# Kernel tuning notes

Hardware: AMD Instinct MI355X
Metric: run time of the kernel (lower is better)

Reference implementation:

```python
import jax, jax.numpy as jnp
import numpy as np

H = 512  # hidden_size


def setup_inputs() -> dict:
    key = jax.random.key(0)
    ks = jax.random.split(key, 8)
    B, L_tgt, L_src = 4, 32, 1024
    query = jax.random.normal(ks[0], (B, L_tgt, H), dtype=jnp.float32)
    states = jax.random.normal(ks[1], (B, L_src, 2 * H), dtype=jnp.float32)
    source_mask = jnp.ones((B, L_src), dtype=jnp.int32)
    s = 0.02
    Wq = jax.random.normal(ks[2], (H, 2 * H), dtype=jnp.float32) * s      # _linear_query.weight^T
    bq = jax.random.normal(ks[3], (2 * H,), dtype=jnp.float32) * s        # _linear_query.bias
    Ws = jax.random.normal(ks[4], (2 * H, 2 * H), dtype=jnp.float32) * s  # _linear_source.weight^T (no bias)
    v = jax.random.normal(ks[5], (2 * H,), dtype=jnp.float32) * s         # _v.weight (no bias)
    Wc = jax.random.normal(ks[6], (3 * H, H), dtype=jnp.float32) * s      # _context.weight^T
    bc = jax.random.normal(ks[7], (H,), dtype=jnp.float32) * s            # _context.bias
    return {"query": query, "states": states, "source_mask": source_mask,
            "Wq": Wq, "bq": bq, "Ws": Ws, "v": v, "Wc": Wc, "bc": bc}


def reference(query, states, source_mask, Wq, bq, Ws, v, Wc, bc):
    # Bahdanau additive attention.
    # query: (B, T, H), states: (B, S, 2H), source_mask: (B, S)
    qf = query @ Wq + bq                         # (B, T, 2H)
    sf = states @ Ws                             # (B, S, 2H)
    # alignments: v . tanh(qf[:, :, None] + sf[:, None, :])  -> (B, T, S)
    feats = jnp.tanh(qf[:, :, None, :] + sf[:, None, :, :])  # (B, T, S, 2H)
    alignments = jnp.einsum('btsd,d->bts', feats, v)
    # mask (B, S) -> (B, 1, S); masked positions get -inf before softmax
    alignments = jnp.where(source_mask[:, None, :].astype(bool), alignments, -jnp.inf)
    attentions = jax.nn.softmax(alignments, axis=2)           # (B, T, S)
    context = jnp.einsum('bts,bsd->btd', attentions, states)  # (B, T, 2H)
    concat_context = jnp.concatenate((context, query), axis=2)  # (B, T, 3H)
    attention_hidden = concat_context @ Wc + bc               # (B, T, H)
    attentions_t = jnp.swapaxes(attentions, 1, 2)             # (B, S, T)
    return (context, attention_hidden, attentions_t)
```

## Files before the change

kernel.cpp:

```cpp
#include <hip/hip_runtime.h>
#include <math.h>


typedef unsigned short u16;
typedef __bf16 bf16x8 __attribute__((ext_vector_type(8)));
typedef float floatx4 __attribute__((ext_vector_type(4)));

#define B_ 4
#define T_ 32
#define S_ 1024
#define H_ 512
#define D_ 1024
#define BT_ 128
#define TWO_LOG2E 2.8853900817779268f

__device__ __forceinline__ float bf2f(u16 u) {
  unsigned int i = ((unsigned int)u) << 16;
  return __builtin_bit_cast(float, i);
}
__device__ __forceinline__ u16 f2bf(float f) {
  unsigned int i = __builtin_bit_cast(unsigned int, f);
  i += 0x7fffu + ((i >> 16) & 1u);
  return (u16)(i >> 16);
}
__device__ __forceinline__ void ld_g2l_16(const u16* g, u16* l) {
  __builtin_amdgcn_global_load_lds((__attribute__((address_space(1))) void*)(u16*)g,
                                   (__attribute__((address_space(3))) void*)l, 16, 0, 0);
}


__global__ __launch_bounds__(256) void prep_fused(const float* __restrict__ states, const float* __restrict__ Ws,
                                                  const float* __restrict__ query, const float* __restrict__ Wq,
                                                  const float* __restrict__ bq,
                                                  u16* __restrict__ sbf, u16* __restrict__ sbfT,
                                                  u16* __restrict__ WsT, float* __restrict__ qf) {
  __shared__ u16 tile[32][65];
  __shared__ float q[8][128];
  const int t = threadIdx.x;
  if (blockIdx.x < 512) {
    const int n0 = (blockIdx.x & 15) * 64, k0 = (blockIdx.x >> 4) * 32;
    const int kr = t >> 3, nc = (t & 7) * 8;
    const float* p = Ws + (size_t)(k0 + kr) * D_ + n0 + nc;
    float4 a = *(const float4*)p, b = *(const float4*)(p + 4);
    tile[kr][nc + 0] = f2bf(a.x); tile[kr][nc + 1] = f2bf(a.y);
    tile[kr][nc + 2] = f2bf(a.z); tile[kr][nc + 3] = f2bf(a.w);
    tile[kr][nc + 4] = f2bf(b.x); tile[kr][nc + 5] = f2bf(b.y);
    tile[kr][nc + 6] = f2bf(b.z); tile[kr][nc + 7] = f2bf(b.w);
    __syncthreads();
    const int nr = t >> 2, kc = (t & 3) * 8;
    union { uint4 v; u16 s[8]; } st;
#pragma unroll
    for (int i = 0; i < 8; ++i) st.s[i] = tile[kc + i][nr];
    *(uint4*)(WsT + (size_t)(n0 + nr) * D_ + k0 + kc) = st.v;
  } else if (blockIdx.x < 2560) {
    const int bid = blockIdx.x - 512;
    const int b = bid >> 9;
    const int r2 = bid & 511;
    const int d0 = (r2 & 15) * 64, s0 = (r2 >> 4) * 32;
    const int sr = t >> 3, dc = (t & 7) * 8;
    const float* p = states + ((size_t)b * S_ + s0 + sr) * D_ + d0 + dc;
    float4 a = *(const float4*)p, bb = *(const float4*)(p + 4);
    union { uint4 v; u16 s[8]; } pk;
    pk.s[0] = f2bf(a.x); pk.s[1] = f2bf(a.y); pk.s[2] = f2bf(a.z); pk.s[3] = f2bf(a.w);
    pk.s[4] = f2bf(bb.x); pk.s[5] = f2bf(bb.y); pk.s[6] = f2bf(bb.z); pk.s[7] = f2bf(bb.w);
    *(uint4*)(sbf + ((size_t)b * S_ + s0 + sr) * D_ + d0 + dc) = pk.v;
#pragma unroll
    for (int i = 0; i < 8; ++i) tile[sr][dc + i] = pk.s[i];
    __syncthreads();
    const int dr = t >> 2, sc = (t & 3) * 8;
    union { uint4 v; u16 s[8]; } st;
#pragma unroll
    for (int i = 0; i < 8; ++i) st.s[i] = tile[sc + i][dr];
    *(uint4*)(sbfT + ((size_t)b * D_ + d0 + dr) * S_ + s0 + sc) = st.v;
  } else {
    const int idx = blockIdx.x - 2560;
    const int c0 = (idx & 3) * 256, r0 = ((idx >> 2) & 15) * 8, k0 = (idx >> 6) * 128;
    for (int i = t; i < 8 * 128; i += 256) {
      const int rl = i >> 7, kk = i & 127;
      q[rl][kk] = query[(size_t)(r0 + rl) * H_ + k0 + kk];
    }
    __syncthreads();
    const int col = c0 + t;
    float acc[8] = {};
    for (int kk = 0; kk < 128; ++kk) {
      const float w = Wq[(size_t)(k0 + kk) * D_ + col];
#pragma unroll
      for (int r = 0; r < 8; ++r) acc[r] = fmaf(q[r][kk], w, acc[r]);
    }
    const float bb = (k0 == 0) ? bq[col] : 0.f;
#pragma unroll
    for (int r = 0; r < 8; ++r)
      atomicAdd(&qf[(size_t)(r0 + r) * D_ + col], TWO_LOG2E * (acc[r] + bb));
  }
}

__global__ __launch_bounds__(256) void f2e_sfgemm(const u16* __restrict__ A, const u16* __restrict__ BT,
                                                  u16* __restrict__ Cb) {
  __shared__ __align__(16) u16 sA[128 * 64];
  __shared__ __align__(16) u16 sB[64 * 64];
  const int bm0 = blockIdx.y * 128, bn0 = blockIdx.x * 64;
  const int t = threadIdx.x;
  const int wv = t >> 6, lane = t & 63;
  const int wm = (wv >> 1) * 64, wn = (wv & 1) * 32;
  const int fm = lane & 15, fq = lane >> 4;
  const int srow = lane >> 3, sp = lane & 7;

  floatx4 acc[4][2];
  const floatx4 fz = {0.f, 0.f, 0.f, 0.f};
#pragma unroll
  for (int i = 0; i < 4; ++i) { acc[i][0] = fz; acc[i][1] = fz; }

  for (int k0 = 0; k0 < D_; k0 += 64) {
    __syncthreads();
#pragma unroll
    for (int j = 0; j < 4; ++j) {
      const int r = wv * 32 + j * 8 + srow;
      const int c = sp ^ (r & 7);
      ld_g2l_16(A + (size_t)(bm0 + r) * D_ + k0 + c * 8, &sA[(wv * 32 + j * 8) * 64]);
    }
#pragma unroll
    for (int j = 0; j < 2; ++j) {
      const int r = wv * 16 + j * 8 + srow;
      const int c = sp ^ (r & 7);
      ld_g2l_16(BT + (size_t)(bn0 + r) * D_ + k0 + c * 8, &sB[(wv * 16 + j * 8) * 64]);
    }
    __syncthreads();
#pragma unroll
    for (int win = 0; win < 2; ++win) {
      bf16x8 af[4], bfr[2];
#pragma unroll
      for (int i = 0; i < 4; ++i) {
        const int R = wm + i * 16 + fm;
        af[i] = *(const bf16x8*)&sA[R * 64 + ((win * 4 + fq) ^ (R & 7)) * 8];
      }
#pragma unroll
      for (int j = 0; j < 2; ++j) {
        const int R = wn + j * 16 + fm;
        bfr[j] = *(const bf16x8*)&sB[R * 64 + ((win * 4 + fq) ^ (R & 7)) * 8];
      }
#pragma unroll
      for (int i = 0; i < 4; ++i)
#pragma unroll
        for (int j = 0; j < 2; ++j)
          acc[i][j] = __builtin_amdgcn_mfma_f32_16x16x32_bf16(af[i], bfr[j], acc[i][j], 0, 0, 0);
    }
  }
#pragma unroll
  for (int i = 0; i < 4; ++i)
#pragma unroll
    for (int j = 0; j < 2; ++j)
#pragma unroll
      for (int r = 0; r < 4; ++r) {
        const int row = bm0 + wm + i * 16 + fq * 4 + r;
        const int col = bn0 + wn + j * 16 + fm;
        Cb[(size_t)row * D_ + col] = f2bf(TWO_LOG2E * acc[i][j][r]);
      }
}

__global__ __launch_bounds__(256, 6) void f3f_align(const float* __restrict__ qf, const u16* __restrict__ sfb,
                                                    const float* __restrict__ v, float* __restrict__ alg) {
  const int wid = (blockIdx.x * 256 + threadIdx.x) >> 6;
  const int lane = threadIdx.x & 63;
  const int b = wid >> 10, s = wid & 1023;
  const int t0 = blockIdx.y * 16;
  float vr[16], sr[16];
  {
    union { uint4 v[2]; u16 s[16]; } u;
    const uint4* sp = (const uint4*)(sfb + (size_t)wid * D_ + lane * 16);
    u.v[0] = sp[0]; u.v[1] = sp[1];
    const float* vp = v + lane * 16;
#pragma unroll
    for (int c = 0; c < 4; ++c) {
      float4 w = *(const float4*)(vp + 4 * c);
      vr[4 * c + 0] = w.x; vr[4 * c + 1] = w.y; vr[4 * c + 2] = w.z; vr[4 * c + 3] = w.w;
    }
#pragma unroll
    for (int j = 0; j < 16; ++j) sr[j] = bf2f(u.s[j]);
  }
  float sum[16];
#pragma unroll
  for (int tt = 0; tt < 16; ++tt) sum[tt] = 0.f;

  const float* qbase = qf + ((size_t)(b * T_ + t0)) * D_ + lane * 16;
  for (int tt = 0; tt < 16; ++tt) {
    const float4* qp = (const float4*)(qbase + (size_t)tt * D_);
    float acc = 0.f;
#pragma unroll
    for (int c = 0; c < 4; ++c) {
      float4 q4 = qp[c];
      float xs[4] = {q4.x, q4.y, q4.z, q4.w};
#pragma unroll
      for (int u2 = 0; u2 < 4; ++u2) {
        const int j = 4 * c + u2;
        const float x = xs[u2] + sr[j];
        const float e = __builtin_amdgcn_exp2f(x);
        acc = fmaf(vr[j], fmaf(-2.f, __builtin_amdgcn_rcpf(e + 1.f), 1.f), acc);
      }
    }
    sum[tt] = acc;
  }
#pragma unroll
  for (int off = 32; off > 0; off >>= 1)
#pragma unroll
    for (int tt = 0; tt < 16; ++tt) sum[tt] += __shfl_xor(sum[tt], off);
  if (lane == 0) {
#pragma unroll
    for (int tt = 0; tt < 16; ++tt)
      alg[((size_t)(b * T_ + t0 + tt)) * S_ + s] = sum[tt];
  }
}

__global__ __launch_bounds__(256) void f4b_softmax(const float* __restrict__ alg, const int* __restrict__ mask,
                                                   float* __restrict__ out_at, u16* __restrict__ pbf) {
  const int r = blockIdx.x;
  const int b = r >> 5, t = r & 31;
  const int tid = threadIdx.x;
  __shared__ float red[256];
  float a[4];
#pragma unroll
  for (int jj = 0; jj < 4; ++jj) {
    const int s = tid + 256 * jj;
    const float x = alg[(size_t)r * S_ + s];
    a[jj] = (mask[(size_t)b * S_ + s] != 0) ? x : -3.0e38f;
  }
  float m = fmaxf(fmaxf(a[0], a[1]), fmaxf(a[2], a[3]));
  red[tid] = m; __syncthreads();
  for (int st = 128; st > 0; st >>= 1) { if (tid < st) red[tid] = fmaxf(red[tid], red[tid + st]); __syncthreads(); }
  m = red[0]; __syncthreads();
  float e[4], lsum = 0.f;
#pragma unroll
  for (int jj = 0; jj < 4; ++jj) {
    e[jj] = (a[jj] > -1.0e38f) ? expf(a[jj] - m) : 0.f;
    lsum += e[jj];
  }
  red[tid] = lsum; __syncthreads();
  for (int st = 128; st > 0; st >>= 1) { if (tid < st) red[tid] += red[tid + st]; __syncthreads(); }
  const float rs = 1.f / red[0];
#pragma unroll
  for (int jj = 0; jj < 4; ++jj) {
    const int s = tid + 256 * jj;
    const float p = e[jj] * rs;
    out_at[((size_t)b * S_ + s) * T_ + t] = p;
    pbf[(size_t)r * S_ + s] = f2bf(p);
  }
}

__global__ __launch_bounds__(256) void f5c_context(const u16* __restrict__ pbf, const u16* __restrict__ sbfT,
                                                   float* __restrict__ ctx) {
  const int b = blockIdx.x >> 4, dt = blockIdx.x & 15;
  const int wv = threadIdx.x >> 6, lane = threadIdx.x & 63;
  const int n0 = dt * 64 + wv * 16;
  const int fm = lane & 15, fq = lane >> 4;
  const floatx4 fz = {0.f, 0.f, 0.f, 0.f};
  floatx4 acc0 = fz, acc1 = fz;
  const u16* pa0 = pbf + ((size_t)b * T_ + fm) * S_ + fq * 8;
  const u16* pa1 = pbf + ((size_t)b * T_ + 16 + fm) * S_ + fq * 8;
  const u16* pb  = sbfT + ((size_t)b * D_ + n0 + fm) * S_ + fq * 8;
#pragma unroll 4
  for (int k0 = 0; k0 < S_; k0 += 32) {
    bf16x8 a0 = *(const bf16x8*)(pa0 + k0);
    bf16x8 a1 = *(const bf16x8*)(pa1 + k0);
    bf16x8 bb = *(const bf16x8*)(pb + k0);
    acc0 = __builtin_amdgcn_mfma_f32_16x16x32_bf16(a0, bb, acc0, 0, 0, 0);
    acc1 = __builtin_amdgcn_mfma_f32_16x16x32_bf16(a1, bb, acc1, 0, 0, 0);
  }
  const int col = n0 + fm;
#pragma unroll
  for (int r = 0; r < 4; ++r) {
    ctx[((size_t)b * T_ + fq * 4 + r) * D_ + col] = acc0[r];
    ctx[((size_t)b * T_ + 16 + fq * 4 + r) * D_ + col] = acc1[r];
  }
}

__global__ __launch_bounds__(256) void f6b_outproj(const float* __restrict__ ctx, const float* __restrict__ query,
                                                   const float* __restrict__ Wc, const float* __restrict__ bc,
                                                   float* __restrict__ out_hid) {
  __shared__ float cq[16][128];
  const int c0 = blockIdx.x * 128, r0 = blockIdx.y * 16, k0 = blockIdx.z * 128;
  const int tid = threadIdx.x;
  const int cl = tid & 127, rh = tid >> 7;
  for (int i = tid; i < 16 * 128; i += 256) {
    const int rl = i >> 7, kk = i & 127;
    const int k = k0 + kk, row = r0 + rl;
    cq[rl][kk] = (k < D_) ? ctx[(size_t)row * D_ + k] : query[(size_t)row * H_ + k - D_];
  }
  __syncthreads();
  float acc[8] = {};
  for (int kk = 0; kk < 128; ++kk) {
    const float w = Wc[(size_t)(k0 + kk) * H_ + c0 + cl];
#pragma unroll
    for (int rr = 0; rr < 8; ++rr) acc[rr] = fmaf(cq[rh * 8 + rr][kk], w, acc[rr]);
  }
  const float bb = (blockIdx.z == 0) ? bc[c0 + cl] : 0.f;
#pragma unroll
  for (int rr = 0; rr < 8; ++rr)
    atomicAdd(&out_hid[(size_t)(r0 + rh * 8 + rr) * H_ + c0 + cl], acc[rr] + bb);
}


__global__ __launch_bounds__(256) void kc_cvt(const float* __restrict__ in, u16* __restrict__ out) {
  const size_t i0 = ((size_t)blockIdx.x * 256 + threadIdx.x) * 8;
  float4 a = *(const float4*)(in + i0);
  float4 b = *(const float4*)(in + i0 + 4);
  union { uint4 v; u16 s[8]; } r;
  r.s[0] = f2bf(a.x); r.s[1] = f2bf(a.y); r.s[2] = f2bf(a.z); r.s[3] = f2bf(a.w);
  r.s[4] = f2bf(b.x); r.s[5] = f2bf(b.y); r.s[6] = f2bf(b.z); r.s[7] = f2bf(b.w);
  *(uint4*)(out + i0) = r.v;
}

__global__ __launch_bounds__(256) void f0_transpose(const float* __restrict__ Ws, u16* __restrict__ WsT) {
  __shared__ u16 tile[32][65];
  const int n0 = blockIdx.x * 64, k0 = blockIdx.y * 32;
  const int t = threadIdx.x;
  {
    const int kr = t >> 3, nc = (t & 7) * 8;
    const float* p = Ws + (size_t)(k0 + kr) * D_ + n0 + nc;
    float4 a = *(const float4*)p, b = *(const float4*)(p + 4);
    tile[kr][nc + 0] = f2bf(a.x); tile[kr][nc + 1] = f2bf(a.y);
    tile[kr][nc + 2] = f2bf(a.z); tile[kr][nc + 3] = f2bf(a.w);
    tile[kr][nc + 4] = f2bf(b.x); tile[kr][nc + 5] = f2bf(b.y);
    tile[kr][nc + 6] = f2bf(b.z); tile[kr][nc + 7] = f2bf(b.w);
  }
  __syncthreads();
  {
    const int nr = t >> 2, kc = (t & 3) * 8;
    union { uint4 v; u16 s[8]; } st;
#pragma unroll
    for (int i = 0; i < 8; ++i) st.s[i] = tile[kc + i][nr];
    *(uint4*)(WsT + (size_t)(n0 + nr) * D_ + k0 + kc) = st.v;
  }
}

__global__ __launch_bounds__(256) void f1b_qf(const float* __restrict__ query, const float* __restrict__ Wq,
                                              const float* __restrict__ bq, float* __restrict__ qf) {
  __shared__ float q[8][128];
  const int c0 = blockIdx.x * 256, r0 = blockIdx.y * 8, k0 = blockIdx.z * 128;
  const int tid = threadIdx.x;
  for (int i = tid; i < 8 * 128; i += 256) {
    const int rl = i >> 7, kk = i & 127;
    q[rl][kk] = query[(size_t)(r0 + rl) * H_ + k0 + kk];
  }
  __syncthreads();
  const int col = c0 + tid;
  float acc[8] = {};
  for (int kk = 0; kk < 128; ++kk) {
    const float w = Wq[(size_t)(k0 + kk) * D_ + col];
#pragma unroll
    for (int r = 0; r < 8; ++r) acc[r] = fmaf(q[r][kk], w, acc[r]);
  }
  const float bb = (blockIdx.z == 0) ? bq[col] : 0.f;
#pragma unroll
  for (int r = 0; r < 8; ++r)
    atomicAdd(&qf[(size_t)(r0 + r) * D_ + col], TWO_LOG2E * (acc[r] + bb));
}

__global__ __launch_bounds__(256) void f2c_sfgemm(const u16* __restrict__ A, const u16* __restrict__ BT,
                                                  u16* __restrict__ Cb) {
  __shared__ __align__(16) u16 sA[128 * 40];
  __shared__ __align__(16) u16 sB[64 * 40];
  const int bm0 = blockIdx.y * 128, bn0 = blockIdx.x * 64;
  const int t = threadIdx.x;
  const int wv = t >> 6, lane = t & 63;
  const int wm = (wv >> 1) * 64, wn = (wv & 1) * 32;
  const int fm = lane & 15, fq = lane >> 4;
  const int arow = t >> 1, akc = (t & 1) * 16;
  const int brow = t >> 2, bkc = (t & 3) * 8;
  floatx4 acc[4][2];
  const floatx4 fz = {0.f, 0.f, 0.f, 0.f};
#pragma unroll
  for (int i = 0; i < 4; ++i) { acc[i][0] = fz; acc[i][1] = fz; }
  const uint4* gA = (const uint4*)(A + (size_t)(bm0 + arow) * D_ + akc);
  const uint4* gB = (const uint4*)(BT + (size_t)(bn0 + brow) * D_ + bkc);
  for (int k0 = 0; k0 < D_; k0 += 32) {
    uint4 va0 = gA[k0 >> 3];
    uint4 va1 = gA[(k0 >> 3) + 1];
    uint4 vb = gB[k0 >> 3];
    __syncthreads();
    *(uint4*)&sA[arow * 40 + akc] = va0;
    *(uint4*)&sA[arow * 40 + akc + 8] = va1;
    *(uint4*)&sB[brow * 40 + bkc] = vb;
    __syncthreads();
    bf16x8 af[4], bfr[2];
#pragma unroll
    for (int i = 0; i < 4; ++i) af[i] = *(const bf16x8*)&sA[(wm + i * 16 + fm) * 40 + fq * 8];
#pragma unroll
    for (int j = 0; j < 2; ++j) bfr[j] = *(const bf16x8*)&sB[(wn + j * 16 + fm) * 40 + fq * 8];
#pragma unroll
    for (int i = 0; i < 4; ++i)
#pragma unroll
      for (int j = 0; j < 2; ++j)
        acc[i][j] = __builtin_amdgcn_mfma_f32_16x16x32_bf16(af[i], bfr[j], acc[i][j], 0, 0, 0);
  }
#pragma unroll
  for (int i = 0; i < 4; ++i)
#pragma unroll
    for (int j = 0; j < 2; ++j)
#pragma unroll
      for (int r = 0; r < 4; ++r) {
        const int row = bm0 + wm + i * 16 + fq * 4 + r;
        const int col = bn0 + wn + j * 16 + fm;
        Cb[(size_t)row * D_ + col] = f2bf(TWO_LOG2E * acc[i][j][r]);
      }
}

__global__ __launch_bounds__(256) void f2d_sfgemm(const float* __restrict__ A, const u16* __restrict__ BT,
                                                  u16* __restrict__ Cb) {
  __shared__ __align__(16) u16 sA[128 * 40];
  __shared__ __align__(16) u16 sB[64 * 40];
  const int bm0 = blockIdx.y * 128, bn0 = blockIdx.x * 64;
  const int t = threadIdx.x;
  const int wv = t >> 6, lane = t & 63;
  const int wm = (wv >> 1) * 64, wn = (wv & 1) * 32;
  const int fm = lane & 15, fq = lane >> 4;
  const int arow = t >> 1, akc = (t & 1) * 16;
  const int brow = t >> 2, bkc = (t & 3) * 8;
  floatx4 acc[4][2];
  const floatx4 fz = {0.f, 0.f, 0.f, 0.f};
#pragma unroll
  for (int i = 0; i < 4; ++i) { acc[i][0] = fz; acc[i][1] = fz; }
  const float* gA = A + (size_t)(bm0 + arow) * D_ + akc;
  const uint4* gB = (const uint4*)(BT + (size_t)(bn0 + brow) * D_ + bkc);
  for (int k0 = 0; k0 < D_; k0 += 32) {
    float4 a0 = *(const float4*)(gA + k0);
    float4 a1 = *(const float4*)(gA + k0 + 4);
    float4 a2 = *(const float4*)(gA + k0 + 8);
    float4 a3 = *(const float4*)(gA + k0 + 12);
    uint4 vb = gB[k0 >> 3];
    union { uint4 v[2]; u16 s[16]; } pa;
    pa.s[0] = f2bf(a0.x); pa.s[1] = f2bf(a0.y); pa.s[2] = f2bf(a0.z); pa.s[3] = f2bf(a0.w);
    pa.s[4] = f2bf(a1.x); pa.s[5] = f2bf(a1.y); pa.s[6] = f2bf(a1.z); pa.s[7] = f2bf(a1.w);
    pa.s[8] = f2bf(a2.x); pa.s[9] = f2bf(a2.y); pa.s[10] = f2bf(a2.z); pa.s[11] = f2bf(a2.w);
    pa.s[12] = f2bf(a3.x); pa.s[13] = f2bf(a3.y); pa.s[14] = f2bf(a3.z); pa.s[15] = f2bf(a3.w);
    __syncthreads();
    *(uint4*)&sA[arow * 40 + akc] = pa.v[0];
    *(uint4*)&sA[arow * 40 + akc + 8] = pa.v[1];
    *(uint4*)&sB[brow * 40 + bkc] = vb;
    __syncthreads();
    bf16x8 af[4], bfr[2];
#pragma unroll
    for (int i = 0; i < 4; ++i) af[i] = *(const bf16x8*)&sA[(wm + i * 16 + fm) * 40 + fq * 8];
#pragma unroll
    for (int j = 0; j < 2; ++j) bfr[j] = *(const bf16x8*)&sB[(wn + j * 16 + fm) * 40 + fq * 8];
#pragma unroll
    for (int i = 0; i < 4; ++i)
#pragma unroll
      for (int j = 0; j < 2; ++j)
        acc[i][j] = __builtin_amdgcn_mfma_f32_16x16x32_bf16(af[i], bfr[j], acc[i][j], 0, 0, 0);
  }
#pragma unroll
  for (int i = 0; i < 4; ++i)
#pragma unroll
    for (int j = 0; j < 2; ++j)
#pragma unroll
      for (int r = 0; r < 4; ++r) {
        const int row = bm0 + wm + i * 16 + fq * 4 + r;
        const int col = bn0 + wn + j * 16 + fm;
        Cb[(size_t)row * D_ + col] = f2bf(TWO_LOG2E * acc[i][j][r]);
      }
}

__global__ __launch_bounds__(256) void f4_softmax(const float* __restrict__ alg, const int* __restrict__ mask,
                                                  float* __restrict__ attn) {
  const int r = blockIdx.x;
  const int b = r >> 5;
  const int tid = threadIdx.x;
  __shared__ float red[256];
  float a[4];
#pragma unroll
  for (int jj = 0; jj < 4; ++jj) {
    const int s = tid + 256 * jj;
    const float x = alg[(size_t)r * S_ + s];
    a[jj] = (mask[(size_t)b * S_ + s] != 0) ? x : -3.0e38f;
  }
  float m = fmaxf(fmaxf(a[0], a[1]), fmaxf(a[2], a[3]));
  red[tid] = m; __syncthreads();
  for (int st = 128; st > 0; st >>= 1) { if (tid < st) red[tid] = fmaxf(red[tid], red[tid + st]); __syncthreads(); }
  m = red[0]; __syncthreads();
  float e[4], lsum = 0.f;
#pragma unroll
  for (int jj = 0; jj < 4; ++jj) {
    e[jj] = (a[jj] > -1.0e38f) ? expf(a[jj] - m) : 0.f;
    lsum += e[jj];
  }
  red[tid] = lsum; __syncthreads();
  for (int st = 128; st > 0; st >>= 1) { if (tid < st) red[tid] += red[tid + st]; __syncthreads(); }
  const float rs = 1.f / red[0];
#pragma unroll
  for (int jj = 0; jj < 4; ++jj)
    attn[(size_t)r * S_ + tid + 256 * jj] = e[jj] * rs;
}

__global__ __launch_bounds__(256) void f5b_context(const float* __restrict__ attn, const u16* __restrict__ sbf,
                                                   float* __restrict__ ctx, float* __restrict__ out_at) {
  __shared__ float at[16][64];
  const int s0 = blockIdx.x * 64, t0 = blockIdx.y * 16, b = blockIdx.z;
  const int tid = threadIdx.x;
  for (int i = tid; i < 16 * 64; i += 256) {
    const int tl = i >> 6, sl = i & 63;
    at[tl][sl] = attn[(size_t)(b * T_ + t0 + tl) * S_ + s0 + sl];
  }
  __syncthreads();
  for (int i = tid; i < 64 * 16; i += 256) {
    const int sl = i >> 4, tl = i & 15;
    out_at[((size_t)b * S_ + s0 + sl) * T_ + t0 + tl] = at[tl][sl];
  }
  float acc[16][4] = {};
  for (int sl = 0; sl < 64; ++sl) {
    const u16* srow = sbf + ((size_t)b * S_ + s0 + sl) * D_ + tid;
    float sv[4];
#pragma unroll
    for (int jj = 0; jj < 4; ++jj) sv[jj] = bf2f(srow[256 * jj]);
#pragma unroll
    for (int tl = 0; tl < 16; ++tl) {
      const float w = at[tl][sl];
#pragma unroll
      for (int jj = 0; jj < 4; ++jj) acc[tl][jj] = fmaf(w, sv[jj], acc[tl][jj]);
    }
  }
#pragma unroll
  for (int tl = 0; tl < 16; ++tl)
#pragma unroll
    for (int jj = 0; jj < 4; ++jj)
      atomicAdd(&ctx[(size_t)(b * T_ + t0 + tl) * D_ + tid + 256 * jj], acc[tl][jj]);
}

__global__ __launch_bounds__(256) void f5_context(const float* __restrict__ attn, const float* __restrict__ states,
                                                  float* __restrict__ ctx, float* __restrict__ out_at) {
  __shared__ float at[16][64];
  const int s0 = blockIdx.x * 64, t0 = blockIdx.y * 16, b = blockIdx.z;
  const int tid = threadIdx.x;
  for (int i = tid; i < 16 * 64; i += 256) {
    const int tl = i >> 6, sl = i & 63;
    at[tl][sl] = attn[(size_t)(b * T_ + t0 + tl) * S_ + s0 + sl];
  }
  __syncthreads();
  for (int i = tid; i < 64 * 16; i += 256) {
    const int sl = i >> 4, tl = i & 15;
    out_at[((size_t)b * S_ + s0 + sl) * T_ + t0 + tl] = at[tl][sl];
  }
  float acc[16][4] = {};
  for (int sl = 0; sl < 64; ++sl) {
    const float* srow = states + ((size_t)b * S_ + s0 + sl) * D_ + tid;
    float sv[4];
#pragma unroll
    for (int jj = 0; jj < 4; ++jj) sv[jj] = srow[256 * jj];
#pragma unroll
    for (int tl = 0; tl < 16; ++tl) {
      const float w = at[tl][sl];
#pragma unroll
      for (int jj = 0; jj < 4; ++jj) acc[tl][jj] = fmaf(w, sv[jj], acc[tl][jj]);
    }
  }
#pragma unroll
  for (int tl = 0; tl < 16; ++tl)
#pragma unroll
    for (int jj = 0; jj < 4; ++jj)
      atomicAdd(&ctx[(size_t)(b * T_ + t0 + tl) * D_ + tid + 256 * jj], acc[tl][jj]);
}


__global__ __launch_bounds__(256) void k1_qf(const float* __restrict__ query, const float* __restrict__ Wq,
                                             const float* __restrict__ bq, float* __restrict__ qf) {
  const int r = blockIdx.x;
  const int tid = threadIdx.x;
  __shared__ float q[H_];
  for (int i = tid; i < H_; i += 256) q[i] = query[(size_t)r * H_ + i];
  __syncthreads();
#pragma unroll
  for (int jj = 0; jj < 4; ++jj) {
    const int j = tid + 256 * jj;
    float acc = bq[j];
    for (int k = 0; k < H_; ++k) acc = fmaf(q[k], Wq[(size_t)k * D_ + j], acc);
    qf[(size_t)r * D_ + j] = acc;
  }
}

__global__ __launch_bounds__(256) void k23_align(const float* __restrict__ states, const float* __restrict__ Ws,
                                                 const float* __restrict__ v, const float* __restrict__ qf,
                                                 float* __restrict__ alg) {
  const int b = blockIdx.x >> 6;
  const int s0 = (blockIdx.x & 63) * 16;
  const int tid = threadIdx.x, lane = tid & 63, wv = tid >> 6;
  __shared__ u16 stL[16 * D_];
  __shared__ float vvL[D_];
  __shared__ float red[16 * 4];
  for (int i = tid; i < 16 * D_; i += 256) {
    const int row = i >> 10, col = i & (D_ - 1);
    stL[i] = f2bf(states[((size_t)b * S_ + s0 + row) * D_ + col]);
  }
  for (int i = tid; i < D_; i += 256) vvL[i] = v[i];
  __syncthreads();
  float acc[64];
#pragma unroll
  for (int i = 0; i < 64; ++i) acc[i] = 0.f;
#pragma unroll 4
  for (int k = 0; k < D_; ++k) {
    float wsv[4];
#pragma unroll
    for (int jj = 0; jj < 4; ++jj) wsv[jj] = Ws[(size_t)k * D_ + tid + 256 * jj];
#pragma unroll
    for (int i = 0; i < 16; ++i) {
      const float sv = bf2f(stL[i * D_ + k]);
#pragma unroll
      for (int jj = 0; jj < 4; ++jj) acc[i * 4 + jj] = fmaf(sv, wsv[jj], acc[i * 4 + jj]);
    }
  }
  for (int t = 0; t < T_; ++t) {
    float qv[4];
#pragma unroll
    for (int jj = 0; jj < 4; ++jj) qv[jj] = qf[((size_t)b * T_ + t) * D_ + tid + 256 * jj];
    float part[16];
#pragma unroll
    for (int i = 0; i < 16; ++i) {
      float p = 0.f;
#pragma unroll
      for (int jj = 0; jj < 4; ++jj)
        p = fmaf(vvL[tid + 256 * jj], tanhf(qv[jj] + acc[i * 4 + jj]), p);
      part[i] = p;
    }
#pragma unroll
    for (int i = 0; i < 16; ++i) {
      float x = part[i];
#pragma unroll
      for (int off = 32; off > 0; off >>= 1) x += __shfl_xor(x, off);
      if (lane == 0) red[i * 4 + wv] = x;
    }
    __syncthreads();
    if (tid < 16)
      alg[((size_t)b * T_ + t) * S_ + s0 + tid] =
          red[tid * 4 + 0] + red[tid * 4 + 1] + red[tid * 4 + 2] + red[tid * 4 + 3];
    __syncthreads();
  }
}

__global__ __launch_bounds__(256) void k4_softmax(const float* __restrict__ alg, const int* __restrict__ mask,
                                                  float* __restrict__ attn) {
  const int r = blockIdx.x;
  const int b = r >> 5;
  const int tid = threadIdx.x;
  __shared__ float red[256];
  float a[4];
#pragma unroll
  for (int jj = 0; jj < 4; ++jj) {
    const int s = tid + 256 * jj;
    const float x = alg[(size_t)r * S_ + s];
    a[jj] = (mask[(size_t)b * S_ + s] != 0) ? x : -3.0e38f;
  }
  float m = fmaxf(fmaxf(a[0], a[1]), fmaxf(a[2], a[3]));
  red[tid] = m; __syncthreads();
  for (int st = 128; st > 0; st >>= 1) { if (tid < st) red[tid] = fmaxf(red[tid], red[tid + st]); __syncthreads(); }
  m = red[0]; __syncthreads();
  float e[4], lsum = 0.f;
#pragma unroll
  for (int jj = 0; jj < 4; ++jj) {
    e[jj] = (a[jj] > -1.0e38f) ? expf(a[jj] - m) : 0.f;
    lsum += e[jj];
  }
  red[tid] = lsum; __syncthreads();
  for (int st = 128; st > 0; st >>= 1) { if (tid < st) red[tid] += red[tid + st]; __syncthreads(); }
  const float rs = 1.f / red[0];
#pragma unroll
  for (int jj = 0; jj < 4; ++jj)
    attn[(size_t)r * S_ + tid + 256 * jj] = e[jj] * rs;
}

__global__ __launch_bounds__(256) void k56_ctx_proj(const float* __restrict__ attn, const float* __restrict__ states,
                                                    const float* __restrict__ query, const float* __restrict__ Wc,
                                                    const float* __restrict__ bc,
                                                    float* __restrict__ out_ctx, float* __restrict__ out_hid,
                                                    float* __restrict__ out_at) {
  const int r = blockIdx.x;
  const int b = r >> 5, t = r & (T_ - 1);
  const int tid = threadIdx.x;
  __shared__ float pr[S_];
  __shared__ float cq[D_ + H_];
  for (int s = tid; s < S_; s += 256) pr[s] = attn[(size_t)r * S_ + s];
  __syncthreads();
  for (int s = tid; s < S_; s += 256) out_at[((size_t)b * S_ + s) * T_ + t] = pr[s];
  float acc[4] = {0.f, 0.f, 0.f, 0.f};
  for (int s = 0; s < S_; ++s) {
    const float w = pr[s];
    const float* srow = states + ((size_t)b * S_ + s) * D_ + tid;
#pragma unroll
    for (int jj = 0; jj < 4; ++jj) acc[jj] = fmaf(w, srow[256 * jj], acc[jj]);
  }
#pragma unroll
  for (int jj = 0; jj < 4; ++jj) {
    cq[tid + 256 * jj] = acc[jj];
    out_ctx[(size_t)r * D_ + tid + 256 * jj] = acc[jj];
  }
  for (int i = tid; i < H_; i += 256) cq[D_ + i] = query[(size_t)r * H_ + i];
  __syncthreads();
#pragma unroll
  for (int jj = 0; jj < 2; ++jj) {
    const int n = tid + 256 * jj;
    float h = bc[n];
    for (int k = 0; k < D_ + H_; ++k) h = fmaf(cq[k], Wc[(size_t)k * H_ + n], h);
    out_hid[(size_t)r * H_ + n] = h;
  }
}

extern "C" void kernel_launch(void* const* d_in, const int* in_sizes, int n_in,
                              void* d_out, int out_size, void* d_ws, size_t ws_size,
                              hipStream_t stream) {
  const float* query  = (const float*)d_in[0];
  const float* states = (const float*)d_in[1];
  const int*   mask   = (const int*)d_in[2];
  const float* Wq     = (const float*)d_in[3];
  const float* bq     = (const float*)d_in[4];
  const float* Ws     = (const float*)d_in[5];
  const float* v      = (const float*)d_in[6];
  const float* Wc     = (const float*)d_in[7];
  const float* bc     = (const float*)d_in[8];

  float* A  = (float*)d_out;
  float* Bh = A + (size_t)BT_ * D_;
  float* C  = Bh + (size_t)BT_ * H_;

  char* ws = (char*)d_ws;
  u16*   sfb  = (u16*)(ws + 0);
  u16*   WsT  = (u16*)(ws + 8388608);
  float* alg  = (float*)(ws + 10485760);
  u16*   sbf  = (u16*)(ws + 11010048);
  u16*   sbfT = (u16*)(ws + 19398656);
  u16*   pbf  = (u16*)(ws + 27787264);

  const size_t WS_T1 = 11010048;
  const size_t WS_T2 = 19398656;
  const size_t WS_T3 = 28049408;

  if (ws_size >= WS_T3) {
    (void)hipMemsetAsync(A, 0, (size_t)(BT_ * D_ + BT_ * H_) * 4, stream);
    prep_fused<<<2816, 256, 0, stream>>>(states, Ws, query, Wq, bq, sbf, sbfT, WsT, A);
    f2e_sfgemm<<<dim3(16, 32), 256, 0, stream>>>(sbf, WsT, sfb);
    f3f_align<<<dim3(1024, 2), 256, 0, stream>>>(A, sfb, v, alg);
    f4b_softmax<<<BT_, 256, 0, stream>>>(alg, mask, C, pbf);
    f5c_context<<<64, 256, 0, stream>>>(pbf, sbfT, A);
    f6b_outproj<<<dim3(4, 8, 12), 256, 0, stream>>>(A, query, Wc, bc, Bh);
  } else if (ws_size >= WS_T1) {
    float* attn = alg;
    (void)hipMemsetAsync(A, 0, (size_t)(BT_ * D_ + BT_ * H_) * 4, stream);
    f1b_qf<<<dim3(4, 16, 4), 256, 0, stream>>>(query, Wq, bq, A);
    f0_transpose<<<dim3(16, 32), 256, 0, stream>>>(Ws, WsT);
    const int tier2 = (ws_size >= WS_T2);
    if (tier2) {
      kc_cvt<<<2048, 256, 0, stream>>>(states, sbf);
      f2c_sfgemm<<<dim3(16, 32), 256, 0, stream>>>(sbf, WsT, sfb);
    } else {
      f2d_sfgemm<<<dim3(16, 32), 256, 0, stream>>>(states, WsT, sfb);
    }
    f3f_align<<<dim3(1024, 2), 256, 0, stream>>>(A, sfb, v, C);
    (void)hipMemsetAsync(A, 0, (size_t)BT_ * D_ * 4, stream);
    f4_softmax<<<BT_, 256, 0, stream>>>(C, mask, attn);
    if (tier2)
      f5b_context<<<dim3(16, 2, 4), 256, 0, stream>>>(attn, sbf, A, C);
    else
      f5_context<<<dim3(16, 2, 4), 256, 0, stream>>>(attn, states, A, C);
    f6b_outproj<<<dim3(4, 8, 12), 256, 0, stream>>>(A, query, Wc, bc, Bh);
  } else {
    k1_qf<<<BT_, 256, 0, stream>>>(query, Wq, bq, A);
    k23_align<<<B_ * (S_ / 16), 256, 0, stream>>>(states, Ws, v, A, C);
    k4_softmax<<<BT_, 256, 0, stream>>>(C, mask, A);
    k56_ctx_proj<<<BT_, 256, 0, stream>>>(A, states, query, Wc, bc, A, Bh, C);
  }
}
```

Baseline: 186.3 us.

## Factor tanh into exponentials of query and source features to cut transcendentals

Adds a new top tier that precomputes exp(2*qf) and exp(2*sf) in the prep and GEMM epilogues. The alignment kernel then evaluates tanh(a+b) as 1 - 2/(e^a*e^b+1), so the inner loop needs one multiply and one reciprocal instead of a tanh per (t,s,d) element. This removes most transcendental work from the hot B*T*S*D loop. The cost is storing Es and Eq in fp32 instead of bf16, which needs more workspace and memory traffic, and the exponentials can overflow for large activations. It only runs when the workspace is large enough.

```diff
diff --git a/kernel.cpp b/kernel.cpp
--- a/kernel.cpp
+++ b/kernel.cpp
@@ -26,6 +26,216 @@
 __device__ __forceinline__ void ld_g2l_16(const u16* g, u16* l) {
   __builtin_amdgcn_global_load_lds((__attribute__((address_space(1))) void*)(u16*)g,
                                    (__attribute__((address_space(3))) void*)l, 16, 0, 0);
+}
+
+
+__global__ __launch_bounds__(256) void prep_fused2(const float* __restrict__ states, const float* __restrict__ Ws,
+                                                   const float* __restrict__ query, const float* __restrict__ Wq,
+                                                   const float* __restrict__ bq,
+                                                   u16* __restrict__ sbf, u16* __restrict__ sbfT,
+                                                   u16* __restrict__ WsT, float* __restrict__ Eq) {
+  __shared__ u16 tile[32][65];
+  __shared__ float qq[8 * 512];
+  const int t = threadIdx.x;
+  if (blockIdx.x < 512) {
+    const int n0 = (blockIdx.x & 15) * 64, k0 = (blockIdx.x >> 4) * 32;
+    const int kr = t >> 3, nc = (t & 7) * 8;
+    const float* p = Ws + (size_t)(k0 + kr) * D_ + n0 + nc;
+    float4 a = *(const float4*)p, b = *(const float4*)(p + 4);
+    tile[kr][nc + 0] = f2bf(a.x); tile[kr][nc + 1] = f2bf(a.y);
+    tile[kr][nc + 2] = f2bf(a.z); tile[kr][nc + 3] = f2bf(a.w);
+    tile[kr][nc + 4] = f2bf(b.x); tile[kr][nc + 5] = f2bf(b.y);
+    tile[kr][nc + 6] = f2bf(b.z); tile[kr][nc + 7] = f2bf(b.w);
+    __syncthreads();
+    const int nr = t >> 2, kc = (t & 3) * 8;
+    union { uint4 v; u16 s[8]; } st;
+#pragma unroll
+    for (int i = 0; i < 8; ++i) st.s[i] = tile[kc + i][nr];
+    *(uint4*)(WsT + (size_t)(n0 + nr) * D_ + k0 + kc) = st.v;
+  } else if (blockIdx.x < 2560) {
+    const int bid = blockIdx.x - 512;
+    const int b = bid >> 9;
+    const int r2 = bid & 511;
+    const int d0 = (r2 & 15) * 64, s0 = (r2 >> 4) * 32;
+    const int sr = t >> 3, dc = (t & 7) * 8;
+    const float* p = states + ((size_t)b * S_ + s0 + sr) * D_ + d0 + dc;
+    float4 a = *(const float4*)p, bb = *(const float4*)(p + 4);
+    union { uint4 v; u16 s[8]; } pk;
+    pk.s[0] = f2bf(a.x); pk.s[1] = f2bf(a.y); pk.s[2] = f2bf(a.z); pk.s[3] = f2bf(a.w);
+    pk.s[4] = f2bf(bb.x); pk.s[5] = f2bf(bb.y); pk.s[6] = f2bf(bb.z); pk.s[7] = f2bf(bb.w);
+    *(uint4*)(sbf + ((size_t)b * S_ + s0 + sr) * D_ + d0 + dc) = pk.v;
+#pragma unroll
+    for (int i = 0; i < 8; ++i) tile[sr][dc + i] = pk.s[i];
+    __syncthreads();
+    const int dr = t >> 2, sc = (t & 3) * 8;
+    union { uint4 v; u16 s[8]; } st;
+#pragma unroll
+    for (int i = 0; i < 8; ++i) st.s[i] = tile[sc + i][dr];
+    *(uint4*)(sbfT + ((size_t)b * D_ + d0 + dr) * S_ + s0 + sc) = st.v;
+  } else {
+    const int idx = blockIdx.x - 2560;
+    const int c0 = (idx & 3) * 256, r0 = (idx >> 2) * 8;
+    const float* qsrc = query + (size_t)r0 * H_;
+    for (int i = t; i < 1024; i += 256)
+      ((float4*)qq)[i] = ((const float4*)qsrc)[i];
+    __syncthreads();
+    const int col = c0 + t;
+    float acc[8] = {};
+    for (int kk = 0; kk < 512; kk += 4) {
+      const float w0 = Wq[(size_t)(kk + 0) * D_ + col];
+      const float w1 = Wq[(size_t)(kk + 1) * D_ + col];
+      const float w2 = Wq[(size_t)(kk + 2) * D_ + col];
+      const float w3 = Wq[(size_t)(kk + 3) * D_ + col];
+#pragma unroll
+      for (int r = 0; r < 8; ++r) {
+        const float4 q4 = *(const float4*)&qq[r * 512 + kk];
+        acc[r] = fmaf(q4.x, w0, acc[r]);
+        acc[r] = fmaf(q4.y, w1, acc[r]);
+        acc[r] = fmaf(q4.z, w2, acc[r]);
+        acc[r] = fmaf(q4.w, w3, acc[r]);
+      }
+    }
+    const float bb = bq[col];
+#pragma unroll
+    for (int r = 0; r < 8; ++r)
+      Eq[(size_t)(r0 + r) * D_ + col] = __builtin_amdgcn_exp2f(TWO_LOG2E * (acc[r] + bb));
+  }
+}
+
+__device__ __forceinline__ void f2f_stage(const u16* __restrict__ A, const u16* __restrict__ BT,
+                                          u16* sAb, u16* sBb, int bm0, int bn0, int k0,
+                                          int wv, int srow, int sp) {
+#pragma unroll
+  for (int j = 0; j < 4; ++j) {
+    const int r = wv * 32 + j * 8 + srow;
+    const int c = sp ^ (r & 7);
+    ld_g2l_16(A + (size_t)(bm0 + r) * D_ + k0 + c * 8, sAb + (wv * 32 + j * 8) * 64);
+  }
+#pragma unroll
+  for (int j = 0; j < 2; ++j) {
+    const int r = wv * 16 + j * 8 + srow;
+    const int c = sp ^ (r & 7);
+    ld_g2l_16(BT + (size_t)(bn0 + r) * D_ + k0 + c * 8, sBb + (wv * 16 + j * 8) * 64);
+  }
+}
+
+__device__ __forceinline__ void f2f_compute(const u16* sAb, const u16* sBb,
+                                            int wm, int wn, int fm, int fq, floatx4 (&acc)[4][2]) {
+#pragma unroll
+  for (int win = 0; win < 2; ++win) {
+    bf16x8 af[4], bfr[2];
+#pragma unroll
+    for (int i = 0; i < 4; ++i) {
+      const int R = wm + i * 16 + fm;
+      af[i] = *(const bf16x8*)&sAb[R * 64 + ((win * 4 + fq) ^ (R & 7)) * 8];
+    }
+#pragma unroll
+    for (int j = 0; j < 2; ++j) {
+      const int R = wn + j * 16 + fm;
+      bfr[j] = *(const bf16x8*)&sBb[R * 64 + ((win * 4 + fq) ^ (R & 7)) * 8];
+    }
+#pragma unroll
+    for (int i = 0; i < 4; ++i)
+#pragma unroll
+      for (int j = 0; j < 2; ++j)
+        acc[i][j] = __builtin_amdgcn_mfma_f32_16x16x32_bf16(af[i], bfr[j], acc[i][j], 0, 0, 0);
+  }
+}
+
+__global__ __launch_bounds__(256) void f2f_sfgemm(const u16* __restrict__ A, const u16* __restrict__ BT,
+                                                  float* __restrict__ Es) {
+  __shared__ __align__(16) u16 sA[2][128 * 64];
+  __shared__ __align__(16) u16 sB[2][64 * 64];
+  const int bm0 = blockIdx.y * 128, bn0 = blockIdx.x * 64;
+  const int t = threadIdx.x;
+  const int wv = t >> 6, lane = t & 63;
+  const int wm = (wv >> 1) * 64, wn = (wv & 1) * 32;
+  const int fm = lane & 15, fq = lane >> 4;
+  const int srow = lane >> 3, sp = lane & 7;
+
+  floatx4 acc[4][2];
+  const floatx4 fz = {0.f, 0.f, 0.f, 0.f};
+#pragma unroll
+  for (int i = 0; i < 4; ++i) { acc[i][0] = fz; acc[i][1] = fz; }
+
+  f2f_stage(A, BT, sA[0], sB[0], bm0, bn0, 0, wv, srow, sp);
+#pragma unroll 1
+  for (int k0 = 0; k0 < D_; k0 += 128) {
+    f2f_stage(A, BT, sA[1], sB[1], bm0, bn0, k0 + 64, wv, srow, sp);
+    asm volatile("s_waitcnt vmcnt(6)" ::: "memory");
+    __builtin_amdgcn_s_barrier();
+    f2f_compute(sA[0], sB[0], wm, wn, fm, fq, acc);
+    __builtin_amdgcn_s_barrier();
+    if (k0 + 128 < D_) {
+      f2f_stage(A, BT, sA[0], sB[0], bm0, bn0, k0 + 128, wv, srow, sp);
+      asm volatile("s_waitcnt vmcnt(6)" ::: "memory");
+    } else {
+      asm volatile("s_waitcnt vmcnt(0)" ::: "memory");
+    }
+    __builtin_amdgcn_s_barrier();
+    f2f_compute(sA[1], sB[1], wm, wn, fm, fq, acc);
+    __builtin_amdgcn_s_barrier();
+  }
+#pragma unroll
+  for (int i = 0; i < 4; ++i)
+#pragma unroll
+    for (int j = 0; j < 2; ++j)
+#pragma unroll
+      for (int r = 0; r < 4; ++r) {
+        const int row = bm0 + wm + i * 16 + fq * 4 + r;
+        const int col = bn0 + wn + j * 16 + fm;
+        Es[(size_t)row * D_ + col] = __builtin_amdgcn_exp2f(TWO_LOG2E * acc[i][j][r]);
+      }
+}
+
+__global__ __launch_bounds__(256, 6) void f3g_align(const float* __restrict__ Eq, const float* __restrict__ Es,
+                                                    const float* __restrict__ v, float* __restrict__ alg) {
+  const int wid = (blockIdx.x * 256 + threadIdx.x) >> 6;
+  const int lane = threadIdx.x & 63;
+  const int b = wid >> 10, s = wid & 1023;
+  const int t0 = blockIdx.y * 16;
+  float vm2[16], es[16];
+  float sumv = 0.f;
+  {
+    const float4* sp = (const float4*)(Es + (size_t)wid * D_ + lane * 16);
+    const float4* vp = (const float4*)(v + lane * 16);
+#pragma unroll
+    for (int c = 0; c < 4; ++c) {
+      const float4 e4 = sp[c];
+      es[4 * c + 0] = e4.x; es[4 * c + 1] = e4.y; es[4 * c + 2] = e4.z; es[4 * c + 3] = e4.w;
+      const float4 w4 = vp[c];
+      vm2[4 * c + 0] = -2.f * w4.x; vm2[4 * c + 1] = -2.f * w4.y;
+      vm2[4 * c + 2] = -2.f * w4.z; vm2[4 * c + 3] = -2.f * w4.w;
+      sumv += w4.x + w4.y + w4.z + w4.w;
+    }
+  }
+  float sum[16];
+  const float* qbase = Eq + ((size_t)(b * T_ + t0)) * D_ + lane * 16;
+  for (int tt = 0; tt < 16; ++tt) {
+    const float4* qp = (const float4*)(qbase + (size_t)tt * D_);
+    float acc = sumv;
+#pragma unroll
+    for (int c = 0; c < 4; ++c) {
+      const float4 q4 = qp[c];
+      const float xs[4] = {q4.x, q4.y, q4.z, q4.w};
+#pragma unroll
+      for (int u2 = 0; u2 < 4; ++u2) {
+        const int j = 4 * c + u2;
+        const float e = xs[u2] * es[j];
+        acc = fmaf(vm2[j], __builtin_amdgcn_rcpf(e + 1.f), acc);
+      }
+    }
+    sum[tt] = acc;
+  }
+#pragma unroll
+  for (int off = 32; off > 0; off >>= 1)
+#pragma unroll
+    for (int tt = 0; tt < 16; ++tt) sum[tt] += __shfl_xor(sum[tt], off);
+  if (lane == 0) {
+#pragma unroll
+    for (int tt = 0; tt < 16; ++tt)
+      alg[((size_t)(b * T_ + t0 + tt)) * S_ + s] = sum[tt];
+  }
 }
 
 
@@ -728,8 +938,24 @@
   const size_t WS_T1 = 11010048;
   const size_t WS_T2 = 19398656;
   const size_t WS_T3 = 28049408;
-
-  if (ws_size >= WS_T3) {
+  const size_t WS_T4 = 36962304;
+
+  if (ws_size >= WS_T4) {
+    float* Es4  = (float*)(ws + 0);
+    u16*   WsT4 = (u16*)(ws + 16777216);
+    float* alg4 = (float*)(ws + 18874368);
+    u16*   sbf4 = (u16*)(ws + 19398656);
+    u16*   sbT4 = (u16*)(ws + 27787264);
+    u16*   pbf4 = (u16*)(ws + 36175872);
+    float* Eq4  = (float*)(ws + 36438016);
+    (void)hipMemsetAsync(Bh, 0, (size_t)BT_ * H_ * 4, stream);
+    prep_fused2<<<2624, 256, 0, stream>>>(states, Ws, query, Wq, bq, sbf4, sbT4, WsT4, Eq4);
+    f2f_sfgemm<<<dim3(16, 32), 256, 0, stream>>>(sbf4, WsT4, Es4);
+    f3g_align<<<dim3(1024, 2), 256, 0, stream>>>(Eq4, Es4, v, alg4);
+    f4b_softmax<<<BT_, 256, 0, stream>>>(alg4, mask, C, pbf4);
+    f5c_context<<<64, 256, 0, stream>>>(pbf4, sbT4, A);
+    f6b_outproj<<<dim3(4, 8, 12), 256, 0, stream>>>(A, query, Wc, bc, Bh);
+  } else if (ws_size >= WS_T3) {
     (void)hipMemsetAsync(A, 0, (size_t)(BT_ * D_ + BT_ * H_) * 4, stream);
     prep_fused<<<2816, 256, 0, stream>>>(states, Ws, query, Wq, bq, sbf, sbfT, WsT, A);
     f2e_sfgemm<<<dim3(16, 32), 256, 0, stream>>>(sbf, WsT, sfb);
```

After: 238.0 us. +27.7%, slower.
